# Performance work log

Measured on AMD Instinct MI355X. Metric: run time of the kernel, lower is better.

Reference implementation:

```python
import jax, jax.numpy as jnp
import numpy as np
from functools import partial

IN_DIM = 128
NUM_HEADS = 8
DOWN_DIM = IN_DIM // 2          # 64
HEAD_DIM = DOWN_DIM // NUM_HEADS  # 8
MID = max(1, DOWN_DIM // 16)    # 4 (gate_reduce=16)
DIL = 3
BN_EPS = 1e-5


def conv2d(x, w, padding=0, dilation=1):
    # x: [B,C,H,W], w: [O,I,kh,kw]
    return jax.lax.conv_general_dilated(
        x, w, window_strides=(1, 1),
        padding=[(padding, padding), (padding, padding)],
        rhs_dilation=(dilation, dilation),
        dimension_numbers=("NCHW", "OIHW", "NCHW"))


def batchnorm(x, gamma, beta, mean, var):
    # inference-mode BN over channel dim
    scale = (gamma / jnp.sqrt(var + BN_EPS))[None, :, None, None]
    shift = (beta - mean * gamma / jnp.sqrt(var + BN_EPS))[None, :, None, None]
    return x * scale + shift


def complex_l2_norm(z, eps=1e-6):
    denom = jnp.sqrt(jnp.sum(z.real ** 2 + z.imag ** 2, axis=-1, keepdims=True) + eps)
    return z / denom


def complex_softmax(z):
    return jax.lax.complex(jax.nn.softmax(z.real, axis=-1),
                           jax.nn.softmax(z.imag, axis=-1))


def setup_inputs() -> dict:
    key = jax.random.key(0)
    ks = jax.random.split(key, 6)
    B, H, W = 8, 128, 128
    inp = {}
    inp["x"] = jax.random.normal(ks[0], (B, IN_DIM, H, W), dtype=jnp.float32)
    inp["conv_w"] = jax.random.normal(ks[1], (DOWN_DIM, IN_DIM, 3, 3), dtype=jnp.float32) * 0.02
    inp["bn1_g"] = jnp.ones((DOWN_DIM,), jnp.float32)
    inp["bn1_b"] = jnp.zeros((DOWN_DIM,), jnp.float32)
    inp["bn1_m"] = jnp.zeros((DOWN_DIM,), jnp.float32)
    inp["bn1_v"] = jnp.ones((DOWN_DIM,), jnp.float32)
    inp["cg1_w"] = jax.random.normal(ks[2], (MID, DOWN_DIM, 1, 1), dtype=jnp.float32) * 0.1
    inp["cg1_b"] = jnp.zeros((MID,), jnp.float32)
    inp["cgbn_g"] = jnp.ones((MID,), jnp.float32)
    inp["cgbn_b"] = jnp.zeros((MID,), jnp.float32)
    inp["cgbn_m"] = jnp.zeros((MID,), jnp.float32)
    inp["cgbn_v"] = jnp.ones((MID,), jnp.float32)
    inp["cg2_w"] = jax.random.normal(ks[3], (DOWN_DIM, MID, 1, 1), dtype=jnp.float32) * 0.1
    inp["cg2_b"] = jnp.zeros((DOWN_DIM,), jnp.float32)
    inp["tau"] = jnp.ones((NUM_HEADS, 1, 1), jnp.float32) * (HEAD_DIM ** -0.5)
    return inp


def reference(x, conv_w, bn1_g, bn1_b, bn1_m, bn1_v,
              cg1_w, cg1_b, cgbn_g, cgbn_b, cgbn_m, cgbn_v,
              cg2_w, cg2_b, tau):
    B, C, H, W = x.shape
    # reduce branch: dilated 3x3 conv -> BN -> GELU (exact, matching torch nn.GELU)
    feat = conv2d(x, conv_w, padding=DIL, dilation=DIL)
    feat = batchnorm(feat, bn1_g, bn1_b, bn1_m, bn1_v)
    feat = jax.nn.gelu(feat, approximate=False)

    # q=k=v=g = fft2(feat) (torch computes four identical FFTs; same math)
    F2 = jnp.fft.fft2(feat.astype(jnp.float32), axes=(-2, -1))  # complex64 [B,64,H,W]
    N = H * W
    qkv = F2.reshape(B, NUM_HEADS, HEAD_DIM, N)  # b h d (H W)
    q = complex_l2_norm(qkv)
    k = complex_l2_norm(qkv)
    v = qkv
    # attn: [b,h,d,d] — tiny; contraction over N
    attn = jnp.einsum("bhdn,bhen->bhde", q, jnp.conj(k)) * tau
    attn = complex_softmax(attn)
    out_f = jnp.einsum("bhde,bhen->bhdn", attn, v)
    out_f = out_f.reshape(B, DOWN_DIM, H, W)
    out_f = jnp.abs(jnp.fft.ifft2(out_f, axes=(-2, -1)))

    # gated branch on g = F2
    gr = F2.real
    cg = conv2d(gr, cg1_w) + cg1_b[None, :, None, None]
    cg = batchnorm(cg, cgbn_g, cgbn_b, cgbn_m, cgbn_v)
    cg = jax.nn.gelu(cg, approximate=False)
    cg = conv2d(cg, cg2_w) + cg2_b[None, :, None, None]
    cg = jax.nn.sigmoid(cg)
    gate = cg * F2  # real gate times complex spectrum
    gate = jnp.abs(jnp.fft.ifft2(gate, axes=(-2, -1)))

    y = jnp.concatenate([out_f, gate], axis=1)
    return y + x
```

## Files before the change

kernel.cpp:

```cpp
#include <hip/hip_runtime.h>
#include <hip/hip_bf16.h>
#include <math.h>

#define NB 8
#define CIN 128
#define CDN 64
#define NPIX 16384
#define NHEADS 8
#define HDIM 8

typedef __attribute__((ext_vector_type(8))) short bf16x8;
typedef __attribute__((ext_vector_type(4))) float f32x4;
typedef __attribute__((ext_vector_type(8))) unsigned short u16x8;

struct alignas(8) c2 { float x, y; };

__device__ inline c2 cadd(c2 a, c2 b){ return {a.x+b.x, a.y+b.y}; }
__device__ inline c2 csub(c2 a, c2 b){ return {a.x-b.x, a.y-b.y}; }
__device__ inline c2 cmul(c2 a, c2 b){ return {a.x*b.x - a.y*b.y, a.x*b.y + a.y*b.x}; }
__device__ inline c2 shfl2(c2 v, int m){ return { __shfl_xor(v.x, m, 64), __shfl_xor(v.y, m, 64) }; }
__device__ inline float gelu_exact(float v){ return 0.5f*v*(1.f + erff(v*0.70710678118654752f)); }
__device__ inline unsigned short f2bf(float f){
  __hip_bfloat16 h = __float2bfloat16(f);
  return *reinterpret_cast<unsigned short*>(&h);
}
__device__ inline float bf2f(unsigned short u){ return __uint_as_float((unsigned)u << 16); }

struct Tw { c2 t0; c2 t[6]; };
__device__ inline void tw_init(Tw& w, int t){
  float sn, cs;
  sincosf(-6.283185307179586f * (float)t * (1.f/128.f), &sn, &cs); w.t0 = {cs, sn};
  #pragma unroll
  for (int i = 0; i < 6; ++i) {
    int sp = 32 >> i;
    int j = t & (sp-1);
    sincosf(-3.141592653589793f * (float)j / (float)sp, &sn, &cs);
    w.t[i] = {cs, sn};
  }
}
__device__ inline void fft128_fwd(c2& a, c2& b, int t, const Tw& w){
  c2 s = cadd(a,b), d = csub(a,b);
  a = s; b = cmul(d, w.t0);
  #pragma unroll
  for (int i = 0; i < 6; ++i) {
    int sp = 32 >> i;
    c2 oa = shfl2(a, sp), ob = shfl2(b, sp);
    c2 tw = w.t[i];
    if (t & sp) { a = cmul(csub(oa,a), tw); b = cmul(csub(ob,b), tw); }
    else        { a = cadd(a,oa);           b = cadd(b,ob); }
  }
}
__device__ inline void fft128_inv(c2& a, c2& b, int t, const Tw& w){
  #pragma unroll
  for (int i = 5; i >= 0; --i) {
    int sp = 32 >> i;
    c2 tw = {w.t[i].x, -w.t[i].y};
    c2 oa = shfl2(a, sp), ob = shfl2(b, sp);
    if (t & sp) { a = csub(oa, cmul(a, tw)); b = csub(ob, cmul(b, tw)); }
    else        { a = cadd(a, cmul(oa, tw)); b = cadd(b, cmul(ob, tw)); }
  }
  c2 t0c = {w.t0.x, -w.t0.y};
  c2 wb = cmul(b, t0c);
  b = csub(a, wb);
  a = cadd(a, wb);
}

__device__ inline void gload_lds16(const void* g, void* l){
  __builtin_amdgcn_global_load_lds(
      (const __attribute__((address_space(1))) unsigned int*)g,
      (__attribute__((address_space(3))) unsigned int*)l, 16, 0, 0);
}

__device__ inline int cmapA(int wv, int i){
  if (wv == 0) return i;
  if (wv == 1) return 4 + i;
  if (wv == 2) return i < 2 ? 8 + i : 12 + i;
  if (wv == 3) return 10 + i;
  if (wv < 8) { int a = wv - 4; return i < 2 ? 16 + 2*a + i : 28 - 2*a + i; }
  int a = wv - 8; return i < 2 ? 32 + 2*a + i : 60 - 2*a + i;
}
__device__ inline int cmapB(int wv, int i){
  return i < 2 ? 2*wv + i : 60 - 2*wv + i;
}

__global__ __launch_bounds__(256) void k_prep(const float* __restrict__ x, unsigned short* __restrict__ xT,
                                              const float* __restrict__ w, unsigned short* __restrict__ wP){
  if (blockIdx.x < 512) {
    int b = blockIdx.x >> 6;
    int px = (blockIdx.x & 63)*256 + threadIdx.x;
    const float* xb = x + (size_t)b*CIN*NPIX + px;
    #pragma unroll 2
    for (int ci0 = 0; ci0 < 128; ci0 += 8) {
      u16x8 v;
      #pragma unroll
      for (int j = 0; j < 8; ++j) v[j] = f2bf(xb[(size_t)(ci0+j)*NPIX]);
      int cc = ci0 >> 5;
      *(u16x8*)(xT + (((size_t)(b*4+cc)*NPIX + px)*32 + (ci0 & 31))) = v;
    }
  } else {
    int idx = (blockIdx.x - 512)*256 + threadIdx.x;
    if (idx >= 4*9*64*32) return;
    int cc  = idx / 18432;
    int r   = idx - cc*18432;
    int tap = r / 2048;
    int r2  = r - tap*2048;
    int co  = r2 >> 5;
    int cil = r2 & 31;
    int ci  = cc*32 + cil;
    wP[idx] = f2bf(w[(co*CIN + ci)*9 + tap]);
  }
}

__global__ __launch_bounds__(256) void k_conv(const unsigned short* __restrict__ xT,
    const unsigned short* __restrict__ wP,
    const float* __restrict__ bg, const float* __restrict__ bbeta,
    const float* __restrict__ bm, const float* __restrict__ bv,
    const float* __restrict__ w1,
    unsigned short* __restrict__ feat, float* __restrict__ u){
  __shared__ __align__(16) unsigned short sX[512*32];
  __shared__ float w1s[256];
  const int tid = threadIdx.x;
  const int flat = blockIdx.x + (blockIdx.y << 4) + (blockIdx.z << 7);
  const int half = (flat >> 3) & 1;
  const int tf   = (flat & 7) | ((flat >> 4) << 3);
  const int x0 = (tf & 7) * 16;
  const int y0 = ((tf >> 3) & 7) * 16;
  const int bb = tf >> 6;
  const int coBase = half*32;
  const int wv  = tid >> 6;
  const int l   = tid & 63;
  const int l15 = l & 15;
  const int g   = l >> 4;

  w1s[tid] = w1[tid];

  const bool interior = (x0 >= 16) && (x0 <= 96) && (y0 >= 16) && (y0 <= 96);

  f32x4 acc[2][4];
  #pragma unroll
  for (int m=0;m<2;++m)
    #pragma unroll
    for (int n=0;n<4;++n) acc[m][n] = {0.f,0.f,0.f,0.f};

  const int ko = g*8;

  for (int cc = 0; cc < 4; ++cc) {
    __syncthreads();
    const unsigned short* xcc = xT + ((size_t)(bb*4 + cc))*NPIX*32;
    if (interior) {
      #pragma unroll
      for (int k = 0; k < 8; ++k) {
        int blk = k*4 + wv;
        int idx = blk*64 + l;
        int p = idx >> 2, i = idx & 3;
        int pc = p < 484 ? p : 483;
        int py = pc / 22, px = pc - py*22;
        int gpix = (y0-3+py)*128 + (x0-3+px);
        int sg = i ^ ((p >> 1) & 3);
        const unsigned short* srcp = xcc + (size_t)gpix*32 + sg*8;
        gload_lds16(srcp, (char*)sX + blk*1024);
      }
    } else {
      #pragma unroll
      for (int k = 0; k < 8; ++k) {
        int idx = k*256 + tid;
        int p = idx >> 2, i = idx & 3;
        u16x8 v = {0,0,0,0,0,0,0,0};
        if (p < 484) {
          int py = p / 22, px = p - py*22;
          int gy = y0-3+py, gx = x0-3+px;
          if ((unsigned)gy < 128u && (unsigned)gx < 128u) {
            int sg = i ^ ((p >> 1) & 3);
            v = *(const u16x8*)(xcc + (size_t)(gy*128+gx)*32 + sg*8);
          }
        }
        *(u16x8*)((char*)sX + idx*16) = v;
      }
    }
    __syncthreads();

    const unsigned short* wcc = wP + cc*18432;
    for (int tap = 0; tap < 9; ++tap) {
      int dy = (tap/3)*3, dx = (tap - (tap/3)*3)*3;
      const unsigned short* wt = wcc + tap*2048;
      bf16x8 a[2], b[4];
      #pragma unroll
      for (int m = 0; m < 2; ++m)
        a[m] = *reinterpret_cast<const bf16x8*>(wt + (coBase + m*16 + l15)*32 + ko);
      #pragma unroll
      for (int n = 0; n < 4; ++n) {
        int p = (wv*4 + n + dy)*22 + l15 + dx;
        b[n] = *reinterpret_cast<const bf16x8*>(&sX[p*32 + ((g ^ ((p >> 1) & 3)) << 3)]);
      }
      #pragma unroll
      for (int m = 0; m < 2; ++m)
        #pragma unroll
        for (int n = 0; n < 4; ++n)
          acc[m][n] = __builtin_amdgcn_mfma_f32_16x16x32_bf16(a[m], b[n], acc[m][n], 0, 0, 0);
    }
  }

  float up[4][4];
  #pragma unroll
  for (int n=0;n<4;++n)
    #pragma unroll
    for (int m2=0;m2<4;++m2) up[n][m2] = 0.f;

  #pragma unroll
  for (int m = 0; m < 2; ++m) {
    #pragma unroll
    for (int r = 0; r < 4; ++r) {
      int co = coBase + m*16 + g*4 + r;
      float sc = bg[co] * rsqrtf(bv[co] + 1e-5f);
      float sh = bbeta[co] - bm[co]*sc;
      float wv4[4];
      #pragma unroll
      for (int m2 = 0; m2 < 4; ++m2) wv4[m2] = w1s[m2*64 + co];
      #pragma unroll
      for (int n = 0; n < 4; ++n) {
        int py = wv*4 + n;
        float v = gelu_exact(acc[m][n][r]*sc + sh);
        feat[((size_t)(bb*CDN + co)*128 + (y0+py))*128 + x0 + l15] = f2bf(v);
        #pragma unroll
        for (int m2 = 0; m2 < 4; ++m2) up[n][m2] += wv4[m2]*v;
      }
    }
  }
  #pragma unroll
  for (int n=0;n<4;++n)
    #pragma unroll
    for (int m2=0;m2<4;++m2) {
      up[n][m2] += __shfl_xor(up[n][m2], 16, 64);
      up[n][m2] += __shfl_xor(up[n][m2], 32, 64);
    }
  if (g == 0) {
    #pragma unroll
    for (int n = 0; n < 4; ++n) {
      int py = y0 + wv*4 + n;
      #pragma unroll
      for (int m2 = 0; m2 < 4; ++m2)
        u[((size_t)((bb*2 + half)*4 + m2))*NPIX + py*128 + x0 + l15] = up[n][m2];
    }
  }
}

__global__ __launch_bounds__(512) void k_mid(const unsigned short* __restrict__ feat, float* __restrict__ part,
    const float* __restrict__ u, const float* __restrict__ b1,
    const float* __restrict__ gg, const float* __restrict__ gbeta,
    const float* __restrict__ gm, const float* __restrict__ gv,
    float* __restrict__ mid){
  __shared__ c2 T[64*129];
  int tid = threadIdx.x, wv = tid >> 6, t = tid & 63;

  if (blockIdx.x < 512) {
    int bh = blockIdx.x >> 3, ck = blockIdx.x & 7;
    int b = bh >> 3, h = bh & 7;
    const unsigned short* f = feat + (size_t)(b*CDN + h*HDIM)*NPIX;
    float acc[36];
    #pragma unroll
    for (int i=0;i<36;++i) acc[i]=0.f;
    for (int p = ck*2048 + tid; p < (ck+1)*2048; p += 512) {
      float v[8];
      #pragma unroll
      for (int d=0; d<8; ++d) v[d] = bf2f(f[d*NPIX + p]);
      int i = 0;
      #pragma unroll
      for (int d=0; d<8; ++d)
        #pragma unroll
        for (int e=0; e<=d; ++e) acc[i++] += v[d]*v[e];
    }
    #pragma unroll
    for (int i=0;i<36;++i)
      #pragma unroll
      for (int off=32; off; off>>=1) acc[i] += __shfl_xor(acc[i], off, 64);
    float* red = (float*)T;
    if (t == 0) {
      #pragma unroll
      for (int i=0;i<36;++i) red[wv*36 + i] = acc[i];
    }
    __syncthreads();
    if (tid < 36) {
      float s = 0.f;
      #pragma unroll
      for (int k = 0; k < 8; ++k) s += red[k*36 + tid];
      part[(bh*8+ck)*36 + tid] = s;
    }
    return;
  }

  int ib = blockIdx.x - 512;
  int b = ib >> 2, m = ib & 3;
  Tw w; tw_init(w, t);
  const float* src0 = u + (size_t)((b*2+0)*4+m)*NPIX;
  const float* src1 = u + (size_t)((b*2+1)*4+m)*NPIX;
  c2 ra[16], rb[16];
  #pragma unroll
  for (int i = 0; i < 16; ++i) {
    int y = wv*16 + i;
    ra[i] = {src0[y*128 + t] + src1[y*128 + t], 0.f};
    rb[i] = {src0[y*128 + t + 64] + src1[y*128 + t + 64], 0.f};
  }
  #pragma unroll
  for (int i = 0; i < 16; ++i) fft128_fwd(ra[i], rb[i], t, w);
  c2 ca[16], cb[16];
  if (wv < 4) {
    #pragma unroll
    for (int i = 0; i < 16; ++i) {
      int y = wv*16 + i;
      T[y*129 + t] = ra[i]; T[y*129 + t + 64] = rb[i];
    }
  }
  __syncthreads();
  #pragma unroll
  for (int i = 0; i < 16; ++i) ca[i] = T[t*129 + wv*16 + i];
  __syncthreads();
  if (wv >= 4) {
    #pragma unroll
    for (int i = 0; i < 16; ++i) {
      int y = (wv-4)*16 + i;
      T[y*129 + t] = ra[i]; T[y*129 + t + 64] = rb[i];
    }
  }
  __syncthreads();
  #pragma unroll
  for (int i = 0; i < 16; ++i) cb[i] = T[t*129 + wv*16 + i];
  #pragma unroll
  for (int i = 0; i < 16; ++i) fft128_fwd(ca[i], cb[i], t, w);
  float sc = gg[m]*rsqrtf(gv[m]+1e-5f);
  float sh = gbeta[m] - gm[m]*sc;
  float bb1 = b1[m];
  float* md = mid + (size_t)(b*4+m)*NPIX;
  #pragma unroll
  for (int i = 0; i < 16; ++i) {
    int kx = wv*16 + i;
    md[kx*128 + t]      = gelu_exact((ca[i].x + bb1)*sc + sh);
    md[kx*128 + t + 64] = gelu_exact((cb[i].x + bb1)*sc + sh);
  }
}

__global__ __launch_bounds__(1024) void k_tail(const float* __restrict__ mid, const float* __restrict__ w2,
    const float* __restrict__ b2, unsigned* __restrict__ gPack,
    const unsigned short* __restrict__ feat, const float* __restrict__ part,
    const float* __restrict__ tau, const float* __restrict__ x, float* __restrict__ out){
  __shared__ float S[384];
  int tid = threadIdx.x;

  if (blockIdx.x < 128) {
    if (tid < 256) S[tid] = w2[tid];
    else if (tid < 320) S[tid] = b2[tid - 256];
    __syncthreads();
    int b = blockIdx.x >> 4;
    int k = (blockIdx.x & 15)*1024 + tid;
    const float* md = mid + (size_t)b*4*NPIX + k;
    float m0 = md[0], m1 = md[NPIX], m2 = md[2*NPIX], m3 = md[3*NPIX];
    unsigned* gp = gPack + (size_t)b*32*NPIX + k;
    #pragma unroll 8
    for (int cp = 0; cp < 32; ++cp) {
      float slo = S[256+cp]    + S[cp*4]*m0      + S[cp*4+1]*m1      + S[cp*4+2]*m2      + S[cp*4+3]*m3;
      float shi = S[256+cp+32] + S[(cp+32)*4]*m0 + S[(cp+32)*4+1]*m1 + S[(cp+32)*4+2]*m2 + S[(cp+32)*4+3]*m3;
      slo = 1.f/(1.f+expf(-slo));
      shi = 1.f/(1.f+expf(-shi));
      gp[(size_t)cp*NPIX] = ((unsigned)f2bf(shi) << 16) | (unsigned)f2bf(slo);
    }
    return;
  }

  int idx = blockIdx.x - 128;
  int bh = idx >> 4;
  int b = bh >> 3, h = bh & 7;
  int p = (idx & 15)*1024 + tid;
  if (tid < 36) {
    float s = 0.f;
    #pragma unroll
    for (int k = 0; k < 8; ++k) s += part[(bh*8+k)*36 + tid];
    S[64 + tid] = s;
  }
  __syncthreads();
  if (tid == 0) {
    float G[8][8];
    int c2i=0;
    for (int d=0;d<8;++d) for(int e=0;e<=d;++e){
      float s = S[64 + c2i]; G[d][e]=s; G[e][d]=s; ++c2i;
    }
    float nrm[8];
    for (int d=0;d<8;++d) nrm[d] = sqrtf(16384.f*G[d][d] + 1e-6f);
    float tv = tau[h];
    for (int d=0;d<8;++d) {
      float row[8]; float mx = -1e30f;
      for (int e=0;e<8;++e){ row[e] = tv*16384.f*G[d][e]/(nrm[d]*nrm[e]); mx = fmaxf(mx,row[e]); }
      float s=0.f;
      for (int e=0;e<8;++e){ row[e] = expf(row[e]-mx); s += row[e]; }
      for (int e=0;e<8;++e) S[d*8+e] = row[e]/s;
    }
  }
  __syncthreads();
  const unsigned short* f = feat + (size_t)(b*CDN + h*HDIM)*NPIX;
  float v[8];
  #pragma unroll
  for (int e=0;e<8;++e) v[e] = bf2f(f[e*NPIX + p]);
  float im = 0.f;
  #pragma unroll
  for (int e=0;e<8;++e) im += v[e];
  im *= 0.125f;
  #pragma unroll
  for (int d=0;d<8;++d){
    float re = 0.f;
    #pragma unroll
    for (int e=0;e<8;++e) re += S[d*8+e]*v[e];
    size_t o = ((size_t)(b*CIN + h*HDIM + d))*NPIX + p;
    out[o] = sqrtf(re*re + im*im) + x[o];
  }
}

__global__ __launch_bounds__(1024)
void k_fused(const unsigned short* __restrict__ feat, const unsigned* __restrict__ gPack,
             const float* __restrict__ x, float* __restrict__ out){
  __shared__ c2 T[128*65];
  int ib = blockIdx.x;
  int b = ib >> 5, c = ib & 31;
  int tid = threadIdx.x, wv = tid >> 6, t = tid & 63;
  Tw w; tw_init(w, t);
  int ta = __brev((64 - (__brev(t) >> 26)) & 63) >> 26;
  const unsigned short* srcA = feat + (size_t)(b*CDN + c)*NPIX;
  const unsigned short* srcB = feat + (size_t)(b*CDN + c + 32)*NPIX;
  const unsigned* gp = gPack + (size_t)(b*32 + c)*NPIX;

  c2 ra[8], rb[8];
  #pragma unroll
  for (int i = 0; i < 8; ++i) {
    int y = wv*8 + i;
    ra[i] = {bf2f(srcA[y*128 + t]),      bf2f(srcB[y*128 + t])};
    rb[i] = {bf2f(srcA[y*128 + t + 64]), bf2f(srcB[y*128 + t + 64])};
  }
  #pragma unroll
  for (int i = 0; i < 8; ++i) fft128_fwd(ra[i], rb[i], t, w);

  #define GUN(w_, lo_, hi_) float lo_ = __uint_as_float((w_) << 16); float hi_ = __uint_as_float((w_) & 0xffff0000u);
  #define CPAIR(I, J) { \
    GUN(gwa[I], g1aI, g2aI); GUN(gwb[I], g1bI, g2bI); \
    GUN(gwa[J], g1aJ, g2aJ); GUN(gwb[J], g1bJ, g2bJ); \
    c2 paI = { __shfl(ca[J].x, ta, 64), -__shfl(ca[J].y, ta, 64) }; \
    c2 paJ = { __shfl(ca[I].x, ta, 64), -__shfl(ca[I].y, ta, 64) }; \
    c2 pbI = { __shfl_xor(cb[J].x, 63, 64), -__shfl_xor(cb[J].y, 63, 64) }; \
    c2 pbJ = { __shfl_xor(cb[I].x, 63, 64), -__shfl_xor(cb[I].y, 63, 64) }; \
    float gsaI=0.5f*(g1aI+g2aI), gdaI=0.5f*(g1aI-g2aI); \
    float gsaJ=0.5f*(g1aJ+g2aJ), gdaJ=0.5f*(g1aJ-g2aJ); \
    float gsbI=0.5f*(g1bI+g2bI), gdbI=0.5f*(g1bI-g2bI); \
    float gsbJ=0.5f*(g1bJ+g2bJ), gdbJ=0.5f*(g1bJ-g2bJ); \
    ca[I] = { gsaI*ca[I].x + gdaI*paI.x, gsaI*ca[I].y + gdaI*paI.y }; \
    ca[J] = { gsaJ*ca[J].x + gdaJ*paJ.x, gsaJ*ca[J].y + gdaJ*paJ.y }; \
    cb[I] = { gsbI*cb[I].x + gdbI*pbI.x, gsbI*cb[I].y + gdbI*pbI.y }; \
    cb[J] = { gsbJ*cb[J].x + gdbJ*pbJ.x, gsbJ*cb[J].y + gdbJ*pbJ.y }; \
  }
  #define CSELF(I) { \
    GUN(gwa[I], g1aI, g2aI); GUN(gwb[I], g1bI, g2bI); \
    c2 paI = { __shfl(ca[I].x, ta, 64), -__shfl(ca[I].y, ta, 64) }; \
    c2 pbI = { __shfl_xor(cb[I].x, 63, 64), -__shfl_xor(cb[I].y, 63, 64) }; \
    float gsaI=0.5f*(g1aI+g2aI), gdaI=0.5f*(g1aI-g2aI); \
    float gsbI=0.5f*(g1bI+g2bI), gdbI=0.5f*(g1bI-g2bI); \
    ca[I] = { gsaI*ca[I].x + gdaI*paI.x, gsaI*ca[I].y + gdaI*paI.y }; \
    cb[I] = { gsbI*cb[I].x + gdbI*pbI.x, gsbI*cb[I].y + gdbI*pbI.y }; \
  }

  #pragma unroll
  for (int i = 0; i < 8; ++i) T[(wv*8 + i)*65 + t] = ra[i];
  __syncthreads();
  {
    int s0 = cmapA(wv,0), s1 = cmapA(wv,1), s2 = cmapA(wv,2), s3 = cmapA(wv,3);
    c2 ca[4], cb[4];
    ca[0]=T[t*65+s0]; ca[1]=T[t*65+s1]; ca[2]=T[t*65+s2]; ca[3]=T[t*65+s3];
    cb[0]=T[(t+64)*65+s0]; cb[1]=T[(t+64)*65+s1]; cb[2]=T[(t+64)*65+s2]; cb[3]=T[(t+64)*65+s3];
    unsigned gwa[4], gwb[4];
    gwa[0]=gp[s0*128+t]; gwa[1]=gp[s1*128+t]; gwa[2]=gp[s2*128+t]; gwa[3]=gp[s3*128+t];
    gwb[0]=gp[s0*128+64+t]; gwb[1]=gp[s1*128+64+t]; gwb[2]=gp[s2*128+64+t]; gwb[3]=gp[s3*128+64+t];
    #pragma unroll
    for (int j = 0; j < 4; ++j) fft128_fwd(ca[j], cb[j], t, w);
    if (wv == 0) { CSELF(0); CSELF(1); CPAIR(2,3); }
    else         { CPAIR(0,3); CPAIR(1,2); }
    #pragma unroll
    for (int j = 0; j < 4; ++j) fft128_inv(ca[j], cb[j], t, w);
    __syncthreads();
    T[t*65+s0]=ca[0]; T[t*65+s1]=ca[1]; T[t*65+s2]=ca[2]; T[t*65+s3]=ca[3];
    T[(t+64)*65+s0]=cb[0]; T[(t+64)*65+s1]=cb[1]; T[(t+64)*65+s2]=cb[2]; T[(t+64)*65+s3]=cb[3];
  }
  __syncthreads();
  #pragma unroll
  for (int i = 0; i < 8; ++i) ra[i] = T[(wv*8 + i)*65 + t];
  __syncthreads();

  #pragma unroll
  for (int i = 0; i < 8; ++i) T[(wv*8 + i)*65 + t] = rb[i];
  __syncthreads();
  {
    int s0 = cmapB(wv,0), s1 = cmapB(wv,1), s2 = cmapB(wv,2), s3 = cmapB(wv,3);
    c2 ca[4], cb[4];
    ca[0]=T[t*65+s0]; ca[1]=T[t*65+s1]; ca[2]=T[t*65+s2]; ca[3]=T[t*65+s3];
    cb[0]=T[(t+64)*65+s0]; cb[1]=T[(t+64)*65+s1]; cb[2]=T[(t+64)*65+s2]; cb[3]=T[(t+64)*65+s3];
    unsigned gwa[4], gwb[4];
    gwa[0]=gp[(64+s0)*128+t]; gwa[1]=gp[(64+s1)*128+t]; gwa[2]=gp[(64+s2)*128+t]; gwa[3]=gp[(64+s3)*128+t];
    gwb[0]=gp[(64+s0)*128+64+t]; gwb[1]=gp[(64+s1)*128+64+t]; gwb[2]=gp[(64+s2)*128+64+t]; gwb[3]=gp[(64+s3)*128+64+t];
    #pragma unroll
    for (int j = 0; j < 4; ++j) fft128_fwd(ca[j], cb[j], t, w);
    CPAIR(0,3); CPAIR(1,2);
    #pragma unroll
    for (int j = 0; j < 4; ++j) fft128_inv(ca[j], cb[j], t, w);
    __syncthreads();
    T[t*65+s0]=ca[0]; T[t*65+s1]=ca[1]; T[t*65+s2]=ca[2]; T[t*65+s3]=ca[3];
    T[(t+64)*65+s0]=cb[0]; T[(t+64)*65+s1]=cb[1]; T[(t+64)*65+s2]=cb[2]; T[(t+64)*65+s3]=cb[3];
  }
  __syncthreads();
  #pragma unroll
  for (int i = 0; i < 8; ++i) rb[i] = T[(wv*8 + i)*65 + t];
  #undef CPAIR
  #undef CSELF
  #undef GUN

  #pragma unroll
  for (int i = 0; i < 8; ++i) fft128_inv(ra[i], rb[i], t, w);
  const float* xr1 = x + ((size_t)(b*CIN + 64 + c))*NPIX;
  const float* xr2 = x + ((size_t)(b*CIN + 96 + c))*NPIX;
  float* o1 = out + ((size_t)(b*CIN + 64 + c))*NPIX;
  float* o2 = out + ((size_t)(b*CIN + 96 + c))*NPIX;
  const float s = 1.f/16384.f;
  #pragma unroll
  for (int i = 0; i < 8; ++i) {
    int y = wv*8 + i;
    o1[y*128 + t]      = fabsf(ra[i].x)*s + xr1[y*128 + t];
    o1[y*128 + t + 64] = fabsf(rb[i].x)*s + xr1[y*128 + t + 64];
    o2[y*128 + t]      = fabsf(ra[i].y)*s + xr2[y*128 + t];
    o2[y*128 + t + 64] = fabsf(rb[i].y)*s + xr2[y*128 + t + 64];
  }
}

extern "C" void kernel_launch(void* const* d_in, const int* in_sizes, int n_in,
                              void* d_out, int out_size, void* d_ws, size_t ws_size,
                              hipStream_t stream){
  const float* x      = (const float*)d_in[0];
  const float* conv_w = (const float*)d_in[1];
  const float* bn1_g  = (const float*)d_in[2];
  const float* bn1_b  = (const float*)d_in[3];
  const float* bn1_m  = (const float*)d_in[4];
  const float* bn1_v  = (const float*)d_in[5];
  const float* cg1_w  = (const float*)d_in[6];
  const float* cg1_b  = (const float*)d_in[7];
  const float* cgbn_g = (const float*)d_in[8];
  const float* cgbn_b = (const float*)d_in[9];
  const float* cgbn_m = (const float*)d_in[10];
  const float* cgbn_v = (const float*)d_in[11];
  const float* cg2_w  = (const float*)d_in[12];
  const float* cg2_b  = (const float*)d_in[13];
  const float* tau    = (const float*)d_in[14];
  float* out = (float*)d_out;

  char* ws = (char*)d_ws;
  unsigned short* feat  = (unsigned short*)ws;
  unsigned short* xT    = (unsigned short*)(ws + 33554432);
  unsigned*       gPack = (unsigned*)(ws + 33554432);
  float*          u     = (float*)(ws + 67108864);
  float*          mid   = (float*)(ws + 71303168);
  unsigned short* wPack = (unsigned short*)(ws + 73400320);
  float*          part  = (float*)(ws + 73547776);

  k_prep<<<800, 256, 0, stream>>>(x, xT, conv_w, wPack);
  k_conv<<<dim3(16,8,NB), 256, 0, stream>>>(xT, wPack, bn1_g, bn1_b, bn1_m, bn1_v, cg1_w, feat, u);
  k_mid<<<544, 512, 0, stream>>>(feat, part, u, cg1_b, cgbn_g, cgbn_b, cgbn_m, cgbn_v, mid);
  k_tail<<<1152, 1024, 0, stream>>>(mid, cg2_w, cg2_b, gPack, feat, part, tau, x, out);
  k_fused<<<NB*32, 1024, 0, stream>>>(feat, gPack, x, out);
}
```

Baseline: 199.5 us.

## Replace shuffle-based FFTs in k_fused with fp16 MFMA DFT matrix multiplies

The gated branch's 2D forward and inverse FFTs in k_fused are rewritten as dense 128-point DFT matrix products on fp16 MFMA units. The DFT twiddle matrix is precomputed by k_prep, and data is staged in XOR-swizzled LDS buffers. k_mid now writes the gate in natural (non-bit-reversed) order to match. The goal is to move FFT arithmetic off shuffle-heavy scalar code onto matrix cores, at the cost of many more FLOPs and reduced fp16 precision for the spectrum values.

```diff
diff --git a/kernel.cpp b/kernel.cpp
--- a/kernel.cpp
+++ b/kernel.cpp
@@ -12,6 +12,8 @@
 typedef __attribute__((ext_vector_type(8))) short bf16x8;
 typedef __attribute__((ext_vector_type(4))) float f32x4;
 typedef __attribute__((ext_vector_type(8))) unsigned short u16x8;
+typedef _Float16 f16x8 __attribute__((ext_vector_type(8)));
+typedef int i32x4 __attribute__((ext_vector_type(4)));
 
 struct alignas(8) c2 { float x, y; };
 
@@ -25,6 +27,11 @@
   return *reinterpret_cast<unsigned short*>(&h);
 }
 __device__ inline float bf2f(unsigned short u){ return __uint_as_float((unsigned)u << 16); }
+__device__ inline f16x8 negh(f16x8 v){
+  i32x4 u = *reinterpret_cast<i32x4*>(&v);
+  u = u ^ (int)0x80008000;
+  return *reinterpret_cast<f16x8*>(&u);
+}
 
 struct Tw { c2 t0; c2 t[6]; };
 __device__ inline void tw_init(Tw& w, int t){
@@ -50,20 +57,6 @@
     else        { a = cadd(a,oa);           b = cadd(b,ob); }
   }
 }
-__device__ inline void fft128_inv(c2& a, c2& b, int t, const Tw& w){
-  #pragma unroll
-  for (int i = 5; i >= 0; --i) {
-    int sp = 32 >> i;
-    c2 tw = {w.t[i].x, -w.t[i].y};
-    c2 oa = shfl2(a, sp), ob = shfl2(b, sp);
-    if (t & sp) { a = csub(oa, cmul(a, tw)); b = csub(ob, cmul(b, tw)); }
-    else        { a = cadd(a, cmul(oa, tw)); b = cadd(b, cmul(ob, tw)); }
-  }
-  c2 t0c = {w.t0.x, -w.t0.y};
-  c2 wb = cmul(b, t0c);
-  b = csub(a, wb);
-  a = cadd(a, wb);
-}
 
 __device__ inline void gload_lds16(const void* g, void* l){
   __builtin_amdgcn_global_load_lds(
@@ -71,20 +64,9 @@
       (__attribute__((address_space(3))) unsigned int*)l, 16, 0, 0);
 }
 
-__device__ inline int cmapA(int wv, int i){
-  if (wv == 0) return i;
-  if (wv == 1) return 4 + i;
-  if (wv == 2) return i < 2 ? 8 + i : 12 + i;
-  if (wv == 3) return 10 + i;
-  if (wv < 8) { int a = wv - 4; return i < 2 ? 16 + 2*a + i : 28 - 2*a + i; }
-  int a = wv - 8; return i < 2 ? 32 + 2*a + i : 60 - 2*a + i;
-}
-__device__ inline int cmapB(int wv, int i){
-  return i < 2 ? 2*wv + i : 60 - 2*wv + i;
-}
-
 __global__ __launch_bounds__(256) void k_prep(const float* __restrict__ x, unsigned short* __restrict__ xT,
-                                              const float* __restrict__ w, unsigned short* __restrict__ wP){
+                                              const float* __restrict__ w, unsigned short* __restrict__ wP,
+                                              _Float16* __restrict__ Wf){
   if (blockIdx.x < 512) {
     int b = blockIdx.x >> 6;
     int px = (blockIdx.x & 63)*256 + threadIdx.x;
@@ -97,7 +79,7 @@
       int cc = ci0 >> 5;
       *(u16x8*)(xT + (((size_t)(b*4+cc)*NPIX + px)*32 + (ci0 & 31))) = v;
     }
-  } else {
+  } else if (blockIdx.x < 800) {
     int idx = (blockIdx.x - 512)*256 + threadIdx.x;
     if (idx >= 4*9*64*32) return;
     int cc  = idx / 18432;
@@ -108,6 +90,14 @@
     int cil = r2 & 31;
     int ci  = cc*32 + cil;
     wP[idx] = f2bf(w[(co*CIN + ci)*9 + tap]);
+  } else {
+    int idx = (blockIdx.x - 800)*256 + threadIdx.x;
+    int part = idx >> 14;
+    int j = (idx >> 7) & 127;
+    int k = idx & 127;
+    int m = (j*k) & 127;
+    float ang = -6.283185307179586f * (float)m / 128.f;
+    Wf[idx] = (_Float16)(part ? sinf(ang) : cosf(ang));
   }
 }
 
@@ -330,11 +320,13 @@
   float sh = gbeta[m] - gm[m]*sc;
   float bb1 = b1[m];
   float* md = mid + (size_t)(b*4+m)*NPIX;
+  int ny = 2*(__brev(t) >> 26);
   #pragma unroll
   for (int i = 0; i < 16; ++i) {
     int kx = wv*16 + i;
-    md[kx*128 + t]      = gelu_exact((ca[i].x + bb1)*sc + sh);
-    md[kx*128 + t + 64] = gelu_exact((cb[i].x + bb1)*sc + sh);
+    int nx = (kx < 64) ? (2*(__brev(kx) >> 26)) : (2*(__brev(kx-64) >> 26) + 1);
+    md[nx*128 + ny]     = gelu_exact((ca[i].x + bb1)*sc + sh);
+    md[nx*128 + ny + 1] = gelu_exact((cb[i].x + bb1)*sc + sh);
   }
 }
 
@@ -414,122 +406,137 @@
 
 __global__ __launch_bounds__(1024)
 void k_fused(const unsigned short* __restrict__ feat, const unsigned* __restrict__ gPack,
+             const _Float16* __restrict__ Wf,
              const float* __restrict__ x, float* __restrict__ out){
-  __shared__ c2 T[128*65];
+  __shared__ _Float16 B0[16384];
+  __shared__ _Float16 B1[16384];
+  __shared__ _Float16 B2[16384];
   int ib = blockIdx.x;
   int b = ib >> 5, c = ib & 31;
-  int tid = threadIdx.x, wv = tid >> 6, t = tid & 63;
-  Tw w; tw_init(w, t);
-  int ta = __brev((64 - (__brev(t) >> 26)) & 63) >> 26;
+  int tid = threadIdx.x, wv = tid >> 6, l = tid & 63;
+  int l15 = l & 15, g = l >> 4;
+  int mT2 = wv >> 2, nT2 = wv & 3;
+  const _Float16* Wr = Wf;
+  const _Float16* Wi = Wf + 16384;
   const unsigned short* srcA = feat + (size_t)(b*CDN + c)*NPIX;
   const unsigned short* srcB = feat + (size_t)(b*CDN + c + 32)*NPIX;
   const unsigned* gp = gPack + (size_t)(b*32 + c)*NPIX;
 
-  c2 ra[8], rb[8];
-  #pragma unroll
-  for (int i = 0; i < 8; ++i) {
-    int y = wv*8 + i;
-    ra[i] = {bf2f(srcA[y*128 + t]),      bf2f(srcB[y*128 + t])};
-    rb[i] = {bf2f(srcA[y*128 + t + 64]), bf2f(srcB[y*128 + t + 64])};
-  }
-  #pragma unroll
-  for (int i = 0; i < 8; ++i) fft128_fwd(ra[i], rb[i], t, w);
-
-  #define GUN(w_, lo_, hi_) float lo_ = __uint_as_float((w_) << 16); float hi_ = __uint_as_float((w_) & 0xffff0000u);
-  #define CPAIR(I, J) { \
-    GUN(gwa[I], g1aI, g2aI); GUN(gwb[I], g1bI, g2bI); \
-    GUN(gwa[J], g1aJ, g2aJ); GUN(gwb[J], g1bJ, g2bJ); \
-    c2 paI = { __shfl(ca[J].x, ta, 64), -__shfl(ca[J].y, ta, 64) }; \
-    c2 paJ = { __shfl(ca[I].x, ta, 64), -__shfl(ca[I].y, ta, 64) }; \
-    c2 pbI = { __shfl_xor(cb[J].x, 63, 64), -__shfl_xor(cb[J].y, 63, 64) }; \
-    c2 pbJ = { __shfl_xor(cb[I].x, 63, 64), -__shfl_xor(cb[I].y, 63, 64) }; \
-    float gsaI=0.5f*(g1aI+g2aI), gdaI=0.5f*(g1aI-g2aI); \
-    float gsaJ=0.5f*(g1aJ+g2aJ), gdaJ=0.5f*(g1aJ-g2aJ); \
-    float gsbI=0.5f*(g1bI+g2bI), gdbI=0.5f*(g1bI-g2bI); \
-    float gsbJ=0.5f*(g1bJ+g2bJ), gdbJ=0.5f*(g1bJ-g2bJ); \
-    ca[I] = { gsaI*ca[I].x + gdaI*paI.x, gsaI*ca[I].y + gdaI*paI.y }; \
-    ca[J] = { gsaJ*ca[J].x + gdaJ*paJ.x, gsaJ*ca[J].y + gdaJ*paJ.y }; \
-    cb[I] = { gsbI*cb[I].x + gdbI*pbI.x, gsbI*cb[I].y + gdbI*pbI.y }; \
-    cb[J] = { gsbJ*cb[J].x + gdbJ*pbJ.x, gsbJ*cb[J].y + gdbJ*pbJ.y }; \
-  }
-  #define CSELF(I) { \
-    GUN(gwa[I], g1aI, g2aI); GUN(gwb[I], g1bI, g2bI); \
-    c2 paI = { __shfl(ca[I].x, ta, 64), -__shfl(ca[I].y, ta, 64) }; \
-    c2 pbI = { __shfl_xor(cb[I].x, 63, 64), -__shfl_xor(cb[I].y, 63, 64) }; \
-    float gsaI=0.5f*(g1aI+g2aI), gdaI=0.5f*(g1aI-g2aI); \
-    float gsbI=0.5f*(g1bI+g2bI), gdbI=0.5f*(g1bI-g2bI); \
-    ca[I] = { gsaI*ca[I].x + gdaI*paI.x, gsaI*ca[I].y + gdaI*paI.y }; \
-    cb[I] = { gsbI*cb[I].x + gdbI*pbI.x, gsbI*cb[I].y + gdbI*pbI.y }; \
-  }
-
-  #pragma unroll
-  for (int i = 0; i < 8; ++i) T[(wv*8 + i)*65 + t] = ra[i];
-  __syncthreads();
   {
-    int s0 = cmapA(wv,0), s1 = cmapA(wv,1), s2 = cmapA(wv,2), s3 = cmapA(wv,3);
-    c2 ca[4], cb[4];
-    ca[0]=T[t*65+s0]; ca[1]=T[t*65+s1]; ca[2]=T[t*65+s2]; ca[3]=T[t*65+s3];
-    cb[0]=T[(t+64)*65+s0]; cb[1]=T[(t+64)*65+s1]; cb[2]=T[(t+64)*65+s2]; cb[3]=T[(t+64)*65+s3];
-    unsigned gwa[4], gwb[4];
-    gwa[0]=gp[s0*128+t]; gwa[1]=gp[s1*128+t]; gwa[2]=gp[s2*128+t]; gwa[3]=gp[s3*128+t];
-    gwb[0]=gp[s0*128+64+t]; gwb[1]=gp[s1*128+64+t]; gwb[2]=gp[s2*128+64+t]; gwb[3]=gp[s3*128+64+t];
-    #pragma unroll
-    for (int j = 0; j < 4; ++j) fft128_fwd(ca[j], cb[j], t, w);
-    if (wv == 0) { CSELF(0); CSELF(1); CPAIR(2,3); }
-    else         { CPAIR(0,3); CPAIR(1,2); }
-    #pragma unroll
-    for (int j = 0; j < 4; ++j) fft128_inv(ca[j], cb[j], t, w);
-    __syncthreads();
-    T[t*65+s0]=ca[0]; T[t*65+s1]=ca[1]; T[t*65+s2]=ca[2]; T[t*65+s3]=ca[3];
-    T[(t+64)*65+s0]=cb[0]; T[(t+64)*65+s1]=cb[1]; T[(t+64)*65+s2]=cb[2]; T[(t+64)*65+s3]=cb[3];
-  }
-  __syncthreads();
-  #pragma unroll
-  for (int i = 0; i < 8; ++i) ra[i] = T[(wv*8 + i)*65 + t];
-  __syncthreads();
-
-  #pragma unroll
-  for (int i = 0; i < 8; ++i) T[(wv*8 + i)*65 + t] = rb[i];
-  __syncthreads();
-  {
-    int s0 = cmapB(wv,0), s1 = cmapB(wv,1), s2 = cmapB(wv,2), s3 = cmapB(wv,3);
-    c2 ca[4], cb[4];
-    ca[0]=T[t*65+s0]; ca[1]=T[t*65+s1]; ca[2]=T[t*65+s2]; ca[3]=T[t*65+s3];
-    cb[0]=T[(t+64)*65+s0]; cb[1]=T[(t+64)*65+s1]; cb[2]=T[(t+64)*65+s2]; cb[3]=T[(t+64)*65+s3];
-    unsigned gwa[4], gwb[4];
-    gwa[0]=gp[(64+s0)*128+t]; gwa[1]=gp[(64+s1)*128+t]; gwa[2]=gp[(64+s2)*128+t]; gwa[3]=gp[(64+s3)*128+t];
-    gwb[0]=gp[(64+s0)*128+64+t]; gwb[1]=gp[(64+s1)*128+64+t]; gwb[2]=gp[(64+s2)*128+64+t]; gwb[3]=gp[(64+s3)*128+64+t];
-    #pragma unroll
-    for (int j = 0; j < 4; ++j) fft128_fwd(ca[j], cb[j], t, w);
-    CPAIR(0,3); CPAIR(1,2);
-    #pragma unroll
-    for (int j = 0; j < 4; ++j) fft128_inv(ca[j], cb[j], t, w);
-    __syncthreads();
-    T[t*65+s0]=ca[0]; T[t*65+s1]=ca[1]; T[t*65+s2]=ca[2]; T[t*65+s3]=ca[3];
-    T[(t+64)*65+s0]=cb[0]; T[(t+64)*65+s1]=cb[1]; T[(t+64)*65+s2]=cb[2]; T[(t+64)*65+s3]=cb[3];
-  }
-  __syncthreads();
-  #pragma unroll
-  for (int i = 0; i < 8; ++i) rb[i] = T[(wv*8 + i)*65 + t];
-  #undef CPAIR
-  #undef CSELF
-  #undef GUN
-
-  #pragma unroll
-  for (int i = 0; i < 8; ++i) fft128_inv(ra[i], rb[i], t, w);
+    int f0 = tid * 16;
+    int y = f0 >> 7, e0 = f0 & 127;
+    u16x8 va0 = *(const u16x8*)(srcA + y*128 + e0);
+    u16x8 va1 = *(const u16x8*)(srcA + y*128 + e0 + 8);
+    u16x8 vb0 = *(const u16x8*)(srcB + y*128 + e0);
+    u16x8 vb1 = *(const u16x8*)(srcB + y*128 + e0 + 8);
+    f16x8 ha0, ha1, hb0, hb1;
+    #pragma unroll
+    for (int j = 0; j < 8; ++j) {
+      ha0[j] = (_Float16)bf2f(va0[j]); ha1[j] = (_Float16)bf2f(va1[j]);
+      hb0[j] = (_Float16)bf2f(vb0[j]); hb1[j] = (_Float16)bf2f(vb1[j]);
+    }
+    int kg = e0 >> 3;
+    *(f16x8*)(B0 + y*128 + ((kg       ^ (y & 15)) << 3)) = ha0;
+    *(f16x8*)(B0 + y*128 + (((kg + 1) ^ (y & 15)) << 3)) = ha1;
+    *(f16x8*)(B1 + y*128 + ((kg       ^ (y & 15)) << 3)) = hb0;
+    *(f16x8*)(B1 + y*128 + (((kg + 1) ^ (y & 15)) << 3)) = hb1;
+  }
+  __syncthreads();
+
+  f32x4 acc[2][2];
+
+  #define LDSF(base, row, kc) (*(const f16x8*)((base) + (row)*128 + (((((kc)*4 + g)) ^ ((row) & 15)) << 3)))
+  #define GLBF(base, row, kc) (*(const f16x8*)((base) + (row)*128 + (kc)*32 + (g << 3)))
+
+  #define GSUB(A1P, A2P, ALDS, B1P, B2P, BLDS, NEGA2) do { \
+    _Pragma("unroll") for (int mi=0;mi<2;++mi) _Pragma("unroll") for (int ni=0;ni<2;++ni) \
+      acc[mi][ni] = (f32x4){0.f,0.f,0.f,0.f}; \
+    _Pragma("unroll") for (int kc=0;kc<4;++kc) { \
+      f16x8 fa1[2], fa2[2], fb1[2], fb2[2]; \
+      _Pragma("unroll") for (int mi=0;mi<2;++mi) { int rA = (mT2*2+mi)*16 + l15; \
+        fa1[mi] = (ALDS) ? LDSF(A1P, rA, kc) : GLBF(A1P, rA, kc); \
+        fa2[mi] = (ALDS) ? LDSF(A2P, rA, kc) : GLBF(A2P, rA, kc); \
+        if (NEGA2) fa2[mi] = negh(fa2[mi]); } \
+      _Pragma("unroll") for (int ni=0;ni<2;++ni) { int rB = (nT2*2+ni)*16 + l15; \
+        fb1[ni] = (BLDS) ? LDSF(B1P, rB, kc) : GLBF(B1P, rB, kc); \
+        fb2[ni] = (BLDS) ? LDSF(B2P, rB, kc) : GLBF(B2P, rB, kc); } \
+      _Pragma("unroll") for (int mi=0;mi<2;++mi) _Pragma("unroll") for (int ni=0;ni<2;++ni) { \
+        acc[mi][ni] = __builtin_amdgcn_mfma_f32_16x16x32_f16(fa1[mi], fb1[ni], acc[mi][ni], 0, 0, 0); \
+        acc[mi][ni] = __builtin_amdgcn_mfma_f32_16x16x32_f16(fa2[mi], fb2[ni], acc[mi][ni], 0, 0, 0); } \
+    } } while(0)
+
+  #define STORE_T(dst, SC) do { \
+    _Pragma("unroll") for (int mi=0;mi<2;++mi) _Pragma("unroll") for (int ni=0;ni<2;++ni) \
+      _Pragma("unroll") for (int r=0;r<4;++r) { \
+        int rr = (mT2*2+mi)*16 + g*4 + r; int cl = (nT2*2+ni)*16 + l15; \
+        (dst)[cl*128 + ((((rr >> 3)) ^ (cl & 15)) << 3) + (rr & 7)] = (_Float16)(acc[mi][ni][r] * (SC)); \
+      } } while(0)
+  #define STORE_N(dst, SC) do { \
+    _Pragma("unroll") for (int mi=0;mi<2;++mi) _Pragma("unroll") for (int ni=0;ni<2;++ni) \
+      _Pragma("unroll") for (int r=0;r<4;++r) { \
+        int rr = (mT2*2+mi)*16 + g*4 + r; int cl = (nT2*2+ni)*16 + l15; \
+        (dst)[rr*128 + ((((cl >> 3)) ^ (rr & 15)) << 3) + (cl & 7)] = (_Float16)(acc[mi][ni][r] * (SC)); \
+      } } while(0)
+
+  GSUB(B0, B1, 1, Wr, Wi, 0, 1);  __syncthreads(); STORE_T(B2, 1.f); __syncthreads();
+  GSUB(B0, B1, 1, Wi, Wr, 0, 0);  __syncthreads(); STORE_T(B0, 1.f); __syncthreads();
+  GSUB(Wr, Wi, 0, B2, B0, 1, 1);  __syncthreads(); STORE_T(B1, 1.f/128.f); __syncthreads();
+  GSUB(Wr, Wi, 0, B0, B2, 1, 0);  __syncthreads(); STORE_T(B0, 1.f/128.f); __syncthreads();
+
+  for (int it = tid; it < 63*128 + 130; it += 1024) {
+    int kx, ky;
+    if (it < 8064) { kx = 1 + (it >> 7); ky = it & 127; }
+    else { int j = it - 8064; kx = (j < 65) ? 0 : 64; ky = (j < 65) ? j : (j - 65); }
+    int kx2 = (128 - kx) & 127, ky2 = (128 - ky) & 127;
+    int a1 = kx *128 + (((ky  >> 3) ^ (kx  & 15)) << 3) + (ky  & 7);
+    int a2 = kx2*128 + (((ky2 >> 3) ^ (kx2 & 15)) << 3) + (ky2 & 7);
+    float f1r = (float)B1[a1], f1i = (float)B0[a1];
+    float f2r = (float)B1[a2], f2i = (float)B0[a2];
+    unsigned w1p = gp[kx*128 + ky];
+    unsigned w2p = gp[kx2*128 + ky2];
+    float g1a = bf2f((unsigned short)(w1p & 0xffff)), g2a = bf2f((unsigned short)(w1p >> 16));
+    float g1b = bf2f((unsigned short)(w2p & 0xffff)), g2b = bf2f((unsigned short)(w2p >> 16));
+    float gs1 = 0.5f*(g1a + g2a), gd1 = 0.5f*(g1a - g2a);
+    float gs2 = 0.5f*(g1b + g2b), gd2 = 0.5f*(g1b - g2b);
+    float y1r = gs1*f1r + gd1*f2r, y1i = gs1*f1i - gd1*f2i;
+    float y2r = gs2*f2r + gd2*f1r, y2i = gs2*f2i - gd2*f1i;
+    B1[a1] = (_Float16)y1r; B0[a1] = (_Float16)y1i;
+    B1[a2] = (_Float16)y2r; B0[a2] = (_Float16)y2i;
+  }
+  __syncthreads();
+  GSUB(Wr, Wi, 0, B1, B0, 1, 0);  __syncthreads(); STORE_N(B2, 1.f); __syncthreads();
+  GSUB(Wr, Wi, 0, B0, B1, 1, 1);  __syncthreads(); STORE_N(B0, 1.f); __syncthreads();
   const float* xr1 = x + ((size_t)(b*CIN + 64 + c))*NPIX;
   const float* xr2 = x + ((size_t)(b*CIN + 96 + c))*NPIX;
   float* o1 = out + ((size_t)(b*CIN + 64 + c))*NPIX;
   float* o2 = out + ((size_t)(b*CIN + 96 + c))*NPIX;
-  const float s = 1.f/16384.f;
-  #pragma unroll
-  for (int i = 0; i < 8; ++i) {
-    int y = wv*8 + i;
-    o1[y*128 + t]      = fabsf(ra[i].x)*s + xr1[y*128 + t];
-    o1[y*128 + t + 64] = fabsf(rb[i].x)*s + xr1[y*128 + t + 64];
-    o2[y*128 + t]      = fabsf(ra[i].y)*s + xr2[y*128 + t];
-    o2[y*128 + t + 64] = fabsf(rb[i].y)*s + xr2[y*128 + t + 64];
-  }
+  const float s = 1.f/128.f;
+
+  GSUB(B2, B0, 1, Wr, Wi, 0, 0);
+  #pragma unroll
+  for (int mi=0;mi<2;++mi)
+    #pragma unroll
+    for (int ni=0;ni<2;++ni)
+      #pragma unroll
+      for (int r=0;r<4;++r) {
+        int rr = (mT2*2+mi)*16 + g*4 + r; int cl = (nT2*2+ni)*16 + l15;
+        o1[rr*128 + cl] = fabsf(acc[mi][ni][r]*s) + xr1[rr*128 + cl];
+      }
+  GSUB(B0, B2, 1, Wr, Wi, 0, 1);
+  #pragma unroll
+  for (int mi=0;mi<2;++mi)
+    #pragma unroll
+    for (int ni=0;ni<2;++ni)
+      #pragma unroll
+      for (int r=0;r<4;++r) {
+        int rr = (mT2*2+mi)*16 + g*4 + r; int cl = (nT2*2+ni)*16 + l15;
+        o2[rr*128 + cl] = fabsf(acc[mi][ni][r]*s) + xr2[rr*128 + cl];
+      }
+  #undef GSUB
+  #undef STORE_T
+  #undef STORE_N
+  #undef LDSF
+  #undef GLBF
 }
 
 extern "C" void kernel_launch(void* const* d_in, const int* in_sizes, int n_in,
@@ -560,10 +567,11 @@
   float*          mid   = (float*)(ws + 71303168);
   unsigned short* wPack = (unsigned short*)(ws + 73400320);
   float*          part  = (float*)(ws + 73547776);
-
-  k_prep<<<800, 256, 0, stream>>>(x, xT, conv_w, wPack);
+  _Float16*       Wf    = (_Float16*)(ws + 73621504);
+
+  k_prep<<<928, 256, 0, stream>>>(x, xT, conv_w, wPack, Wf);
   k_conv<<<dim3(16,8,NB), 256, 0, stream>>>(xT, wPack, bn1_g, bn1_b, bn1_m, bn1_v, cg1_w, feat, u);
   k_mid<<<544, 512, 0, stream>>>(feat, part, u, cg1_b, cgbn_g, cgbn_b, cgbn_m, cgbn_v, mid);
   k_tail<<<1152, 1024, 0, stream>>>(mid, cg2_w, cg2_b, gPack, feat, part, tau, x, out);
-  k_fused<<<NB*32, 1024, 0, stream>>>(feat, gPack, x, out);
-}
+  k_fused<<<NB*32, 1024, 0, stream>>>(feat, gPack, Wf, x, out);
+}
```

Result: slower. 217.3 us (+8.9%).
